# Kernel optimization log

Measured on AMD Instinct MI355X. Metric: run time of the kernel, lower is better.

The kernel has to match this reference:

```python
import jax, jax.numpy as jnp
from jax import lax
import numpy as np

D_MODEL = 512
D_INNER = 1024
DT_RANK = 32
D_STATE = 16
D_CONV = 3
B, L = 2, 1024
SQ = 4  # sqrt(d_state)


def setup_inputs() -> dict:
    key = jax.random.key(0)
    ks = jax.random.split(key, 16)
    s = lambda *sh: 1.0 / np.sqrt(sh[-1])
    inp = {
        "x": jax.random.normal(ks[0], (B, L, D_MODEL), jnp.float32),
        "h": jax.random.normal(ks[1], (B, L, D_INNER, D_STATE), jnp.float32),
        "in_proj_w": jax.random.normal(ks[2], (2 * D_INNER, D_MODEL), jnp.float32) * s(D_MODEL),
        "conv1d_w": jax.random.normal(ks[3], (D_INNER, 1, D_CONV), jnp.float32) * 0.3,
        "conv1d_b": jax.random.normal(ks[4], (D_INNER,), jnp.float32) * 0.02,
        "x_proj_w": jax.random.normal(ks[5], (DT_RANK + 2 * D_STATE, D_INNER), jnp.float32) * s(D_INNER),
        "dt_proj_w": jax.random.normal(ks[6], (D_INNER, DT_RANK), jnp.float32) * s(DT_RANK),
        "dt_proj_b": jax.random.normal(ks[7], (D_INNER,), jnp.float32) * 0.1 - 4.0,
        "A_log": jnp.log(jnp.tile(jnp.arange(1, D_STATE + 1, dtype=jnp.float32), (D_INNER, 1))),
        "D": jnp.ones((D_INNER,), jnp.float32),
        "sf1_w": jax.random.normal(ks[8], (D_INNER, 1, 1, 1), jnp.float32) * 0.3,
        "sf1_b": jax.random.normal(ks[9], (D_INNER,), jnp.float32) * 0.02,
        "sf2_w": jax.random.normal(ks[10], (D_INNER, 1, 3, 3), jnp.float32) * 0.3,
        "sf2_b": jax.random.normal(ks[11], (D_INNER,), jnp.float32) * 0.02,
        "alpha": jnp.ones((2,), jnp.float32),
        "out_proj_w": jax.random.normal(ks[12], (D_MODEL, D_INNER), jnp.float32) * s(D_INNER),
    }
    return inp


def _dwconv1d(x_bdl, w, b):
    # x: [B, D, L], w: [D, 1, K], groups=D, SAME padding (K=3, pad=1)
    y = lax.conv_general_dilated(x_bdl, w, (1,), [(1, 1)],
                                 dimension_numbers=("NCH", "OIH", "NCH"),
                                 feature_group_count=D_INNER)
    return y + b[None, :, None]


def _dwconv2d(x, w, b, pad):
    y = lax.conv_general_dilated(x, w, (1, 1), [(pad, pad), (pad, pad)],
                                 dimension_numbers=("NCHW", "OIHW", "NCHW"),
                                 feature_group_count=D_INNER)
    return y + b[None, :, None, None]


def reference(x, h, in_proj_w, conv1d_w, conv1d_b, x_proj_w, dt_proj_w, dt_proj_b,
              A_log, D, sf1_w, sf1_b, sf2_w, sf2_b, alpha, out_proj_w):
    # in_proj -> split x/z
    xz = x @ in_proj_w.T                       # [B, L, 2*Di]
    xc, z = jnp.split(xz, 2, axis=-1)
    # depthwise causal-ish conv1d over L
    xc = _dwconv1d(jnp.transpose(xc, (0, 2, 1)), conv1d_w, conv1d_b)
    xs = jax.nn.silu(jnp.transpose(xc, (0, 2, 1)))  # [B, L, Di]

    # ssm_step
    A = -jnp.exp(A_log)                         # [Di, S]
    dBC = xs @ x_proj_w.T                       # [B, L, R+2S]
    delta, Bm, Cm = jnp.split(dBC, [DT_RANK, DT_RANK + D_STATE], axis=-1)
    delta = jax.nn.softplus(delta @ dt_proj_w.T + dt_proj_b)  # [B, L, Di]
    deltaA = jnp.exp(delta[..., None] * A)      # [B, L, Di, S]
    BX = (delta * xs)[..., None] * Bm[:, :, None, :]
    hn = deltaA * h + BX                        # [B, L, Di, S]

    # state fusion: reshape state dim S into 4x4 spatial, depthwise 1x1 + 3x3 convs
    h2 = hn.reshape(B * L, D_INNER, SQ, SQ)
    hf = alpha[0] * _dwconv2d(h2, sf1_w, sf1_b, 0) + alpha[1] * _dwconv2d(h2, sf2_w, sf2_b, 1)
    hn = hf.reshape(B, L, D_INNER, D_STATE)

    y = jnp.einsum("blds,bls->bld", hn, Cm) + D * xs
    out = (y * jax.nn.silu(z)) @ out_proj_w.T   # [B, L, Dm]
    return out, hn
```

## Files before the change

### kernel.cpp

```cpp
#include <hip/hip_runtime.h>
#include <stdint.h>

#define BLT 2048
#define DMODEL 512
#define DINNER 1024

typedef __bf16 bf16x8 __attribute__((ext_vector_type(8)));
typedef float f32x4 __attribute__((ext_vector_type(4)));

template <int BN>
__global__ __launch_bounds__(256) void gemm_mfma(const float* __restrict__ A,
                                                 const float* __restrict__ B,
                                                 float* __restrict__ C,
                                                 int M, int N, int K) {
    __shared__ __bf16 As[128][72];
    __shared__ __bf16 Bs[BN][72];
    const int tid = threadIdx.x;
    const int wave = tid >> 6, lane = tid & 63;
    const int waveM = wave >> 1, waveN = wave & 1;
    const int quad = lane >> 4, l16 = lane & 15;
    constexpr int WN = BN / 2;
    constexpr int NI = WN / 16;
    const int m0 = blockIdx.y * 128, n0 = blockIdx.x * BN;

    f32x4 acc[4][NI];
#pragma unroll
    for (int mi = 0; mi < 4; mi++)
#pragma unroll
        for (int ni = 0; ni < NI; ni++) acc[mi][ni] = (f32x4){0.f, 0.f, 0.f, 0.f};

    const int sr = tid >> 4;
    const int sc = (tid & 15) * 4;

    for (int k0 = 0; k0 < K; k0 += 64) {
#pragma unroll
        for (int p = 0; p < 8; p++) {
            int r = sr + p * 16;
            float4 v = *(const float4*)(A + (size_t)(m0 + r) * K + k0 + sc);
            union { __bf16 b[4]; uint2 u; } pk;
            pk.b[0] = (__bf16)v.x; pk.b[1] = (__bf16)v.y;
            pk.b[2] = (__bf16)v.z; pk.b[3] = (__bf16)v.w;
            *(uint2*)&As[r][sc] = pk.u;
        }
#pragma unroll
        for (int p = 0; p < BN / 16; p++) {
            int r = sr + p * 16;
            float4 v = *(const float4*)(B + (size_t)(n0 + r) * K + k0 + sc);
            union { __bf16 b[4]; uint2 u; } pk;
            pk.b[0] = (__bf16)v.x; pk.b[1] = (__bf16)v.y;
            pk.b[2] = (__bf16)v.z; pk.b[3] = (__bf16)v.w;
            *(uint2*)&Bs[r][sc] = pk.u;
        }
        __syncthreads();
#pragma unroll
        for (int kk = 0; kk < 64; kk += 32) {
            bf16x8 af[4], bfr[NI];
#pragma unroll
            for (int mi = 0; mi < 4; mi++)
                af[mi] = *(const bf16x8*)&As[waveM * 64 + mi * 16 + l16][kk + quad * 8];
#pragma unroll
            for (int ni = 0; ni < NI; ni++)
                bfr[ni] = *(const bf16x8*)&Bs[waveN * WN + ni * 16 + l16][kk + quad * 8];
#pragma unroll
            for (int mi = 0; mi < 4; mi++)
#pragma unroll
                for (int ni = 0; ni < NI; ni++)
                    acc[mi][ni] = __builtin_amdgcn_mfma_f32_16x16x32_bf16(
                        af[mi], bfr[ni], acc[mi][ni], 0, 0, 0);
        }
        __syncthreads();
    }
#pragma unroll
    for (int mi = 0; mi < 4; mi++)
#pragma unroll
        for (int ni = 0; ni < NI; ni++)
#pragma unroll
            for (int reg = 0; reg < 4; reg++) {
                int m = m0 + waveM * 64 + mi * 16 + quad * 4 + reg;
                int n = n0 + waveN * WN + ni * 16 + l16;
                C[(size_t)m * N + n] = acc[mi][ni][reg];
            }
}

__global__ __launch_bounds__(256) void conv1d_silu_k(const float* __restrict__ xz,
                                                     const float* __restrict__ w,
                                                     const float* __restrict__ bias,
                                                     float* __restrict__ xs) {
    int idx = blockIdx.x * 256 + threadIdx.x;
    int t = idx >> 10, d = idx & 1023;
    int l = t & 1023;
    float cur = xz[(size_t)t * 2048 + d];
    float prev = (l > 0) ? xz[(size_t)(t - 1) * 2048 + d] : 0.f;
    float nxt = (l < 1023) ? xz[(size_t)(t + 1) * 2048 + d] : 0.f;
    float v = w[d * 3] * prev + w[d * 3 + 1] * cur + w[d * 3 + 2] * nxt + bias[d];
    xs[idx] = v / (1.f + __expf(-v));
}

__global__ __launch_bounds__(256) void ssm_fuse_k(
    const float* __restrict__ h,
    const float* __restrict__ xz,
    const float* __restrict__ xs,
    const float* __restrict__ dBC,
    const float* __restrict__ dtw,
    const float* __restrict__ dtb,
    const float* __restrict__ A_log,
    const float* __restrict__ Dp,
    const float* __restrict__ sf1w, const float* __restrict__ sf1b,
    const float* __restrict__ sf2w, const float* __restrict__ sf2b,
    const float* __restrict__ alpha,
    float* __restrict__ hn_out,
    float* __restrict__ yz) {
    const int tid = threadIdx.x;
    const int t = blockIdx.y;
    const int dq = blockIdx.x;
    const int d = dq * 256 + tid;
    __shared__ float dbc_s[64];
    __shared__ float dtw_s[256][33];
    if (tid < 64) dbc_s[tid] = dBC[t * 64 + tid];
    {
        const float* wsrc = dtw + (size_t)dq * 256 * 32;
#pragma unroll
        for (int j = 0; j < 8; j++) {
            int f = tid + j * 256;
            float4 v = *(const float4*)(wsrc + (size_t)f * 4);
            int row = f >> 3, c = (f & 7) * 4;
            dtw_s[row][c] = v.x; dtw_s[row][c + 1] = v.y;
            dtw_s[row][c + 2] = v.z; dtw_s[row][c + 3] = v.w;
        }
    }
    __syncthreads();
    float accd = dtb[d];
#pragma unroll
    for (int r = 0; r < 32; r++) accd += dbc_s[r] * dtw_s[tid][r];
    const float dt = (accd > 20.f) ? accd : __logf(1.f + __expf(accd));

    const size_t td = (size_t)t * 1024 + d;
    const float xv = xs[td];
    const float dx = dt * xv;
    float hv[16], al[16];
    const float4* hp = (const float4*)(h + td * 16);
    const float4* apv = (const float4*)(A_log + (size_t)d * 16);
#pragma unroll
    for (int q = 0; q < 4; q++) {
        float4 hq = hp[q];
        hv[q * 4 + 0] = hq.x; hv[q * 4 + 1] = hq.y; hv[q * 4 + 2] = hq.z; hv[q * 4 + 3] = hq.w;
        float4 aq = apv[q];
        al[q * 4 + 0] = aq.x; al[q * 4 + 1] = aq.y; al[q * 4 + 2] = aq.z; al[q * 4 + 3] = aq.w;
    }
    float hn[16];
#pragma unroll
    for (int s = 0; s < 16; s++) {
        float Av = -__expf(al[s]);
        hn[s] = __expf(dt * Av) * hv[s] + dx * dbc_s[32 + s];
    }
    const float w1 = sf1w[d], b1 = sf1b[d], b2v = sf2b[d];
    const float a0f = alpha[0], a1f = alpha[1];
    float w2[9];
#pragma unroll
    for (int k = 0; k < 9; k++) w2[k] = sf2w[d * 9 + k];
    float hf[16];
#pragma unroll
    for (int i = 0; i < 4; i++)
#pragma unroll
        for (int j = 0; j < 4; j++) {
            float s2 = b2v;
#pragma unroll
            for (int ki = 0; ki < 3; ki++)
#pragma unroll
                for (int kj = 0; kj < 3; kj++) {
                    int ii = i + ki - 1, jj = j + kj - 1;
                    if (ii >= 0 && ii < 4 && jj >= 0 && jj < 4)
                        s2 += hn[ii * 4 + jj] * w2[ki * 3 + kj];
                }
            hf[i * 4 + j] = a0f * (w1 * hn[i * 4 + j] + b1) + a1f * s2;
        }
    float y = Dp[d] * xv;
#pragma unroll
    for (int s = 0; s < 16; s++) y += hf[s] * dbc_s[48 + s];
    const float zv = xz[(size_t)t * 2048 + 1024 + d];
    yz[td] = y * (zv / (1.f + __expf(-zv)));
    float4* op = (float4*)(hn_out + td * 16);
#pragma unroll
    for (int q = 0; q < 4; q++)
        op[q] = make_float4(hf[q * 4 + 0], hf[q * 4 + 1], hf[q * 4 + 2], hf[q * 4 + 3]);
}

extern "C" void kernel_launch(void* const* d_in, const int* in_sizes, int n_in,
                              void* d_out, int out_size, void* d_ws, size_t ws_size,
                              hipStream_t stream) {
    const float* x         = (const float*)d_in[0];
    const float* h         = (const float*)d_in[1];
    const float* in_proj_w = (const float*)d_in[2];
    const float* conv1d_w  = (const float*)d_in[3];
    const float* conv1d_b  = (const float*)d_in[4];
    const float* x_proj_w  = (const float*)d_in[5];
    const float* dt_proj_w = (const float*)d_in[6];
    const float* dt_proj_b = (const float*)d_in[7];
    const float* A_log     = (const float*)d_in[8];
    const float* Dp        = (const float*)d_in[9];
    const float* sf1w      = (const float*)d_in[10];
    const float* sf1b      = (const float*)d_in[11];
    const float* sf2w      = (const float*)d_in[12];
    const float* sf2b      = (const float*)d_in[13];
    const float* alpha     = (const float*)d_in[14];
    const float* out_projw = (const float*)d_in[15];

    float* out0   = (float*)d_out;
    float* hn_out = out0 + (size_t)BLT * DMODEL;

    float* xz  = (float*)d_ws;
    float* xs  = xz + (size_t)BLT * 2048;
    float* dBC = xs + (size_t)BLT * DINNER;
    float* yz  = dBC + (size_t)BLT * 64;

    gemm_mfma<128><<<dim3(2048 / 128, BLT / 128), 256, 0, stream>>>(x, in_proj_w, xz,
                                                                    BLT, 2048, DMODEL);
    conv1d_silu_k<<<(BLT * DINNER) / 256, 256, 0, stream>>>(xz, conv1d_w, conv1d_b, xs);
    gemm_mfma<64><<<dim3(1, BLT / 128), 256, 0, stream>>>(xs, x_proj_w, dBC, BLT, 64, DINNER);
    ssm_fuse_k<<<dim3(4, BLT), 256, 0, stream>>>(h, xz, xs, dBC, dt_proj_w, dt_proj_b,
                                                 A_log, Dp, sf1w, sf1b, sf2w, sf2b, alpha,
                                                 hn_out, yz);
    gemm_mfma<128><<<dim3(DMODEL / 128, BLT / 128), 256, 0, stream>>>(yz, out_projw, out0,
                                                                      BLT, DMODEL, DINNER);
}
```

Measured before the change: 422.2 us.

## Precompute transposed dt weights and negated A, use smaller-tile x_proj GEMM

Adds a prep kernel that transposes dt_proj_w and precomputes -exp(A_log). This removes the per-block 32KB shared-memory staging of dt weights and the per-element exp in ssm_fuse_k, which should raise occupancy there. The x_proj GEMM now runs on a new 32x64-tile kernel, giving 64 blocks instead of 16 so more CUs share that skinny GEMM. The cost is one extra small kernel launch per call, and the dt dot-product now reads the transposed weights from global or cache instead of shared memory.

```diff
diff --git a/kernel.cpp b/kernel.cpp
--- a/kernel.cpp
+++ b/kernel.cpp
@@ -8,26 +8,23 @@
 typedef __bf16 bf16x8 __attribute__((ext_vector_type(8)));
 typedef float f32x4 __attribute__((ext_vector_type(4)));
 
-template <int BN>
 __global__ __launch_bounds__(256) void gemm_mfma(const float* __restrict__ A,
                                                  const float* __restrict__ B,
                                                  float* __restrict__ C,
                                                  int M, int N, int K) {
     __shared__ __bf16 As[128][72];
-    __shared__ __bf16 Bs[BN][72];
+    __shared__ __bf16 Bs[128][72];
     const int tid = threadIdx.x;
     const int wave = tid >> 6, lane = tid & 63;
     const int waveM = wave >> 1, waveN = wave & 1;
     const int quad = lane >> 4, l16 = lane & 15;
-    constexpr int WN = BN / 2;
-    constexpr int NI = WN / 16;
-    const int m0 = blockIdx.y * 128, n0 = blockIdx.x * BN;
-
-    f32x4 acc[4][NI];
+    const int m0 = blockIdx.y * 128, n0 = blockIdx.x * 128;
+
+    f32x4 acc[4][4];
 #pragma unroll
     for (int mi = 0; mi < 4; mi++)
 #pragma unroll
-        for (int ni = 0; ni < NI; ni++) acc[mi][ni] = (f32x4){0.f, 0.f, 0.f, 0.f};
+        for (int ni = 0; ni < 4; ni++) acc[mi][ni] = (f32x4){0.f, 0.f, 0.f, 0.f};
 
     const int sr = tid >> 4;
     const int sc = (tid & 15) * 4;
@@ -43,7 +40,7 @@
             *(uint2*)&As[r][sc] = pk.u;
         }
 #pragma unroll
-        for (int p = 0; p < BN / 16; p++) {
+        for (int p = 0; p < 8; p++) {
             int r = sr + p * 16;
             float4 v = *(const float4*)(B + (size_t)(n0 + r) * K + k0 + sc);
             union { __bf16 b[4]; uint2 u; } pk;
@@ -54,17 +51,17 @@
         __syncthreads();
 #pragma unroll
         for (int kk = 0; kk < 64; kk += 32) {
-            bf16x8 af[4], bfr[NI];
+            bf16x8 af[4], bfr[4];
 #pragma unroll
             for (int mi = 0; mi < 4; mi++)
                 af[mi] = *(const bf16x8*)&As[waveM * 64 + mi * 16 + l16][kk + quad * 8];
 #pragma unroll
-            for (int ni = 0; ni < NI; ni++)
-                bfr[ni] = *(const bf16x8*)&Bs[waveN * WN + ni * 16 + l16][kk + quad * 8];
+            for (int ni = 0; ni < 4; ni++)
+                bfr[ni] = *(const bf16x8*)&Bs[waveN * 64 + ni * 16 + l16][kk + quad * 8];
 #pragma unroll
             for (int mi = 0; mi < 4; mi++)
 #pragma unroll
-                for (int ni = 0; ni < NI; ni++)
+                for (int ni = 0; ni < 4; ni++)
                     acc[mi][ni] = __builtin_amdgcn_mfma_f32_16x16x32_bf16(
                         af[mi], bfr[ni], acc[mi][ni], 0, 0, 0);
         }
@@ -73,13 +70,85 @@
 #pragma unroll
     for (int mi = 0; mi < 4; mi++)
 #pragma unroll
-        for (int ni = 0; ni < NI; ni++)
+        for (int ni = 0; ni < 4; ni++)
 #pragma unroll
             for (int reg = 0; reg < 4; reg++) {
                 int m = m0 + waveM * 64 + mi * 16 + quad * 4 + reg;
-                int n = n0 + waveN * WN + ni * 16 + l16;
+                int n = n0 + waveN * 64 + ni * 16 + l16;
                 C[(size_t)m * N + n] = acc[mi][ni][reg];
             }
+}
+
+__global__ __launch_bounds__(256) void gemm_mfma_s(const float* __restrict__ A,
+                                                   const float* __restrict__ B,
+                                                   float* __restrict__ C,
+                                                   int M, int N, int K) {
+    __shared__ __bf16 As[32][72];
+    __shared__ __bf16 Bs[64][72];
+    const int tid = threadIdx.x;
+    const int wave = tid >> 6, lane = tid & 63;
+    const int waveM = wave >> 1, waveN = wave & 1;
+    const int quad = lane >> 4, l16 = lane & 15;
+    const int m0 = blockIdx.y * 32, n0 = blockIdx.x * 64;
+
+    f32x4 acc[2];
+    acc[0] = (f32x4){0.f, 0.f, 0.f, 0.f};
+    acc[1] = (f32x4){0.f, 0.f, 0.f, 0.f};
+
+    const int sr = tid >> 4;
+    const int sc = (tid & 15) * 4;
+
+    for (int k0 = 0; k0 < K; k0 += 64) {
+#pragma unroll
+        for (int p = 0; p < 2; p++) {
+            int r = sr + p * 16;
+            float4 v = *(const float4*)(A + (size_t)(m0 + r) * K + k0 + sc);
+            union { __bf16 b[4]; uint2 u; } pk;
+            pk.b[0] = (__bf16)v.x; pk.b[1] = (__bf16)v.y;
+            pk.b[2] = (__bf16)v.z; pk.b[3] = (__bf16)v.w;
+            *(uint2*)&As[r][sc] = pk.u;
+        }
+#pragma unroll
+        for (int p = 0; p < 4; p++) {
+            int r = sr + p * 16;
+            float4 v = *(const float4*)(B + (size_t)(n0 + r) * K + k0 + sc);
+            union { __bf16 b[4]; uint2 u; } pk;
+            pk.b[0] = (__bf16)v.x; pk.b[1] = (__bf16)v.y;
+            pk.b[2] = (__bf16)v.z; pk.b[3] = (__bf16)v.w;
+            *(uint2*)&Bs[r][sc] = pk.u;
+        }
+        __syncthreads();
+#pragma unroll
+        for (int kk = 0; kk < 64; kk += 32) {
+            bf16x8 af = *(const bf16x8*)&As[waveM * 16 + l16][kk + quad * 8];
+#pragma unroll
+            for (int ni = 0; ni < 2; ni++) {
+                bf16x8 bf = *(const bf16x8*)&Bs[waveN * 32 + ni * 16 + l16][kk + quad * 8];
+                acc[ni] = __builtin_amdgcn_mfma_f32_16x16x32_bf16(af, bf, acc[ni], 0, 0, 0);
+            }
+        }
+        __syncthreads();
+    }
+#pragma unroll
+    for (int ni = 0; ni < 2; ni++)
+#pragma unroll
+        for (int reg = 0; reg < 4; reg++) {
+            int m = m0 + waveM * 16 + quad * 4 + reg;
+            int n = n0 + waveN * 32 + ni * 16 + l16;
+            C[(size_t)m * N + n] = acc[ni][reg];
+        }
+}
+
+__global__ __launch_bounds__(256) void prep_k(const float* __restrict__ dtw,
+                                              const float* __restrict__ A_log,
+                                              float* __restrict__ dtwT,
+                                              float* __restrict__ Aneg) {
+    int i = blockIdx.x * 256 + threadIdx.x;
+    {
+        int r = i >> 10, d = i & 1023;
+        dtwT[i] = dtw[d * 32 + r];
+    }
+    if (i < 16384) Aneg[i] = -__expf(A_log[i]);
 }
 
 __global__ __launch_bounds__(256) void conv1d_silu_k(const float* __restrict__ xz,
@@ -101,9 +170,9 @@
     const float* __restrict__ xz,
     const float* __restrict__ xs,
     const float* __restrict__ dBC,
-    const float* __restrict__ dtw,
+    const float* __restrict__ dtwT,
     const float* __restrict__ dtb,
-    const float* __restrict__ A_log,
+    const float* __restrict__ Aneg,
     const float* __restrict__ Dp,
     const float* __restrict__ sf1w, const float* __restrict__ sf1b,
     const float* __restrict__ sf2w, const float* __restrict__ sf2b,
@@ -112,47 +181,32 @@
     float* __restrict__ yz) {
     const int tid = threadIdx.x;
     const int t = blockIdx.y;
-    const int dq = blockIdx.x;
-    const int d = dq * 256 + tid;
+    const int d = blockIdx.x * 256 + tid;
     __shared__ float dbc_s[64];
-    __shared__ float dtw_s[256][33];
     if (tid < 64) dbc_s[tid] = dBC[t * 64 + tid];
-    {
-        const float* wsrc = dtw + (size_t)dq * 256 * 32;
-#pragma unroll
-        for (int j = 0; j < 8; j++) {
-            int f = tid + j * 256;
-            float4 v = *(const float4*)(wsrc + (size_t)f * 4);
-            int row = f >> 3, c = (f & 7) * 4;
-            dtw_s[row][c] = v.x; dtw_s[row][c + 1] = v.y;
-            dtw_s[row][c + 2] = v.z; dtw_s[row][c + 3] = v.w;
-        }
-    }
     __syncthreads();
     float accd = dtb[d];
 #pragma unroll
-    for (int r = 0; r < 32; r++) accd += dbc_s[r] * dtw_s[tid][r];
+    for (int r = 0; r < 32; r++) accd += dbc_s[r] * dtwT[r * 1024 + d];
     const float dt = (accd > 20.f) ? accd : __logf(1.f + __expf(accd));
 
     const size_t td = (size_t)t * 1024 + d;
     const float xv = xs[td];
     const float dx = dt * xv;
-    float hv[16], al[16];
+    float hv[16], an[16];
     const float4* hp = (const float4*)(h + td * 16);
-    const float4* apv = (const float4*)(A_log + (size_t)d * 16);
+    const float4* apv = (const float4*)(Aneg + (size_t)d * 16);
 #pragma unroll
     for (int q = 0; q < 4; q++) {
         float4 hq = hp[q];
         hv[q * 4 + 0] = hq.x; hv[q * 4 + 1] = hq.y; hv[q * 4 + 2] = hq.z; hv[q * 4 + 3] = hq.w;
         float4 aq = apv[q];
-        al[q * 4 + 0] = aq.x; al[q * 4 + 1] = aq.y; al[q * 4 + 2] = aq.z; al[q * 4 + 3] = aq.w;
+        an[q * 4 + 0] = aq.x; an[q * 4 + 1] = aq.y; an[q * 4 + 2] = aq.z; an[q * 4 + 3] = aq.w;
     }
     float hn[16];
 #pragma unroll
-    for (int s = 0; s < 16; s++) {
-        float Av = -__expf(al[s]);
-        hn[s] = __expf(dt * Av) * hv[s] + dx * dbc_s[32 + s];
-    }
+    for (int s = 0; s < 16; s++)
+        hn[s] = __expf(dt * an[s]) * hv[s] + dx * dbc_s[32 + s];
     const float w1 = sf1w[d], b1 = sf1b[d], b2v = sf2b[d];
     const float a0f = alpha[0], a1f = alpha[1];
     float w2[9];
@@ -208,18 +262,21 @@
     float* out0   = (float*)d_out;
     float* hn_out = out0 + (size_t)BLT * DMODEL;
 
-    float* xz  = (float*)d_ws;
-    float* xs  = xz + (size_t)BLT * 2048;
-    float* dBC = xs + (size_t)BLT * DINNER;
-    float* yz  = dBC + (size_t)BLT * 64;
-
-    gemm_mfma<128><<<dim3(2048 / 128, BLT / 128), 256, 0, stream>>>(x, in_proj_w, xz,
-                                                                    BLT, 2048, DMODEL);
+    float* xz   = (float*)d_ws;
+    float* xs   = xz + (size_t)BLT * 2048;
+    float* dBC  = xs + (size_t)BLT * DINNER;
+    float* yz   = dBC + (size_t)BLT * 64;
+    float* dtwT = yz + (size_t)BLT * DINNER;
+    float* Aneg = dtwT + 32 * 1024;
+
+    prep_k<<<128, 256, 0, stream>>>(dt_proj_w, A_log, dtwT, Aneg);
+    gemm_mfma<<<dim3(2048 / 128, BLT / 128), 256, 0, stream>>>(x, in_proj_w, xz,
+                                                               BLT, 2048, DMODEL);
     conv1d_silu_k<<<(BLT * DINNER) / 256, 256, 0, stream>>>(xz, conv1d_w, conv1d_b, xs);
-    gemm_mfma<64><<<dim3(1, BLT / 128), 256, 0, stream>>>(xs, x_proj_w, dBC, BLT, 64, DINNER);
-    ssm_fuse_k<<<dim3(4, BLT), 256, 0, stream>>>(h, xz, xs, dBC, dt_proj_w, dt_proj_b,
-                                                 A_log, Dp, sf1w, sf1b, sf2w, sf2b, alpha,
+    gemm_mfma_s<<<dim3(1, BLT / 32), 256, 0, stream>>>(xs, x_proj_w, dBC, BLT, 64, DINNER);
+    ssm_fuse_k<<<dim3(4, BLT), 256, 0, stream>>>(h, xz, xs, dBC, dtwT, dt_proj_b,
+                                                 Aneg, Dp, sf1w, sf1b, sf2w, sf2b, alpha,
                                                  hn_out, yz);
-    gemm_mfma<128><<<dim3(DMODEL / 128, BLT / 128), 256, 0, stream>>>(yz, out_projw, out0,
-                                                                      BLT, DMODEL, DINNER);
-}
+    gemm_mfma<<<dim3(DMODEL / 128, BLT / 128), 256, 0, stream>>>(yz, out_projw, out0,
+                                                                 BLT, DMODEL, DINNER);
+}
```

New measurement: 403.1 us. -4.5%, faster.
